# Performance work log

Measured on AMD Instinct MI355X. Metric: run time of the kernel, lower is better.

## Reference

```python
import jax, jax.numpy as jnp
import numpy as np

NUM_GROUPS = 32
EPS = 1e-5

def group_norm(x, weight, bias):
    # x: [B, C, H, W]
    b, c, h, w = x.shape
    g = NUM_GROUPS
    xg = x.reshape(b, g, (c // g) * h * w)
    mean = xg.mean(axis=-1, keepdims=True)
    var = xg.var(axis=-1, keepdims=True)
    xn = ((xg - mean) * jax.lax.rsqrt(var + EPS)).reshape(b, c, h, w)
    return xn * weight[None, :, None, None] + bias[None, :, None, None]

def setup_inputs() -> dict:
    key = jax.random.key(0)
    ks = jax.random.split(key, 4)
    B, C, H, W = 4, 256, 64, 64
    x = jax.random.normal(ks[0], (B, C, H, W), dtype=jnp.float32)
    gn_weight = jnp.ones((C,), dtype=jnp.float32)
    gn_bias = jnp.zeros((C,), dtype=jnp.float32)
    # 1x1 conv == linear over channel dim; init ~ kaiming-uniform-ish scale
    qkv_weight = jax.random.normal(ks[1], (3 * C, C), dtype=jnp.float32) / np.sqrt(C)
    qkv_bias = jnp.zeros((3 * C,), dtype=jnp.float32)
    out_weight = jax.random.normal(ks[2], (C, C), dtype=jnp.float32) / np.sqrt(C)
    out_bias = jnp.zeros((C,), dtype=jnp.float32)
    return {"x": x, "gn_weight": gn_weight, "gn_bias": gn_bias,
            "qkv_weight": qkv_weight, "qkv_bias": qkv_bias,
            "out_weight": out_weight, "out_bias": out_bias}

def reference(x, gn_weight, gn_bias, qkv_weight, qkv_bias, out_weight, out_bias):
    b, c, h, w = x.shape
    n = h * w
    xn = group_norm(x, gn_weight, gn_bias)
    # 1x1 conv QKV projection: [B, 3C, H, W]
    qkv = jnp.einsum('bchw,oc->bohw', xn, qkv_weight) + qkv_bias[None, :, None, None]
    q, k, v = jnp.split(qkv, 3, axis=1)
    q = q.transpose(0, 2, 3, 1).reshape(b, n, c)   # [B, N, C]
    k = k.reshape(b, c, n)                         # [B, C, N]
    v = v.transpose(0, 2, 3, 1).reshape(b, n, c)   # [B, N, C]
    scores = jnp.einsum('bnc,bcm->bnm', q, k) * (c ** -0.5)  # [B, N, N]
    attn = jax.nn.softmax(scores, axis=-1)
    out = jnp.einsum('bnm,bmc->bnc', attn, v)      # [B, N, C]
    out = out.reshape(b, h, w, c).transpose(0, 3, 1, 2)  # [B, C, H, W]
    out = jnp.einsum('bchw,oc->bohw', out, out_weight) + out_bias[None, :, None, None]
    return out + x
```

## Files before the change

### kernel.cpp

```cpp
#include <hip/hip_runtime.h>
#include <math.h>

#define B_   4
#define C_   256
#define G_   32
#define CPG  8
#define N_   4096
#define NPG  (CPG * N_)
#define EPS  1e-5f
#define SCALE 0.0625f

typedef __attribute__((ext_vector_type(8)))  __bf16 bf16x8;
typedef __attribute__((ext_vector_type(4)))  __bf16 bf16x4;
typedef __attribute__((ext_vector_type(16))) float  f32x16;

__global__ __launch_bounds__(256) void gn_stats_kernel(const float* __restrict__ x,
                                                       float* __restrict__ part) {
    int bid = blockIdx.x;
    int bg = bid >> 2, seg = bid & 3;
    const float4* xp4 = (const float4*)(x + (size_t)bg * NPG) + seg * 2048;
    int tid = threadIdx.x;

    float s = 0.f, ss = 0.f;
    for (int i = tid; i < 2048; i += 256) {
        float4 t = xp4[i];
        s  += t.x + t.y + t.z + t.w;
        ss += t.x * t.x + t.y * t.y + t.z * t.z + t.w * t.w;
    }
    #pragma unroll
    for (int off = 32; off; off >>= 1) {
        s  += __shfl_xor(s, off, 64);
        ss += __shfl_xor(ss, off, 64);
    }
    __shared__ float rs[2][4];
    int wave = tid >> 6, lane = tid & 63;
    if (lane == 0) { rs[0][wave] = s; rs[1][wave] = ss; }
    __syncthreads();
    if (tid == 0) {
        part[bid * 2]     = rs[0][0] + rs[0][1] + rs[0][2] + rs[0][3];
        part[bid * 2 + 1] = rs[1][0] + rs[1][1] + rs[1][2] + rs[1][3];
    }
}

__global__ __launch_bounds__(256) void gn_apply_kernel(const float* __restrict__ x,
                                                       const float* __restrict__ w,
                                                       const float* __restrict__ bia,
                                                       const float* __restrict__ part,
                                                       __bf16* __restrict__ xnb) {
    int bid = blockIdx.x;
    int bg = bid >> 4, seg = bid & 15;
    int b = bg >> 5, g = bg & 31;
    float s  = part[(bg * 4 + 0) * 2] + part[(bg * 4 + 1) * 2]
             + part[(bg * 4 + 2) * 2] + part[(bg * 4 + 3) * 2];
    float ss = part[(bg * 4 + 0) * 2 + 1] + part[(bg * 4 + 1) * 2 + 1]
             + part[(bg * 4 + 2) * 2 + 1] + part[(bg * 4 + 3) * 2 + 1];
    float mean = s / (float)NPG;
    float var  = ss / (float)NPG - mean * mean;
    float rstd = rsqrtf(var + EPS);

    const float* xp = x + (size_t)bg * NPG;
    int n = seg * 256 + threadIdx.x;

    bf16x8 pk;
    #pragma unroll
    for (int cc = 0; cc < 8; cc++) {
        float sc = rstd * w[g * CPG + cc];
        float sh = bia[g * CPG + cc] - mean * sc;
        pk[cc] = (__bf16)(xp[(size_t)cc * N_ + n] * sc + sh);
    }
    size_t idx = ((((size_t)(b * 128 + (n >> 5)) * 16 + (g >> 1)) * 2 + (g & 1))
                  * 32 + (n & 31)) * 8;
    *(bf16x8*)(xnb + idx) = pk;
}

__global__ __launch_bounds__(256) void qkv_kernel(const __bf16* __restrict__ xnb,
                                                  const float* __restrict__ W,
                                                  const float* __restrict__ bias,
                                                  __bf16* __restrict__ q,
                                                  __bf16* __restrict__ k,
                                                  __bf16* __restrict__ v) {
    int b = blockIdx.z, ot = blockIdx.y, nc = blockIdx.x;
    int tid = threadIdx.x, wv = tid >> 6, lane = tid & 63;
    int n31 = lane & 31, q2 = lane >> 5;
    int B0 = ot * 128 + wv * 32;

    bf16x8 wf[16];
    const float* wp = W + (size_t)(B0 + n31) * C_;
    #pragma unroll
    for (int ks = 0; ks < 16; ks++) {
        float4 t0 = *(const float4*)(wp + ks * 16 + q2 * 8);
        float4 t1 = *(const float4*)(wp + ks * 16 + q2 * 8 + 4);
        bf16x8 f;
        f[0] = (__bf16)t0.x; f[1] = (__bf16)t0.y; f[2] = (__bf16)t0.z; f[3] = (__bf16)t0.w;
        f[4] = (__bf16)t1.x; f[5] = (__bf16)t1.y; f[6] = (__bf16)t1.z; f[7] = (__bf16)t1.w;
        wf[ks] = f;
    }

    float bv[16], bvv = 0.f;
    if (ot < 4) {
        #pragma unroll
        for (int gI = 0; gI < 4; gI++)
            #pragma unroll
            for (int j = 0; j < 4; j++)
                bv[gI * 4 + j] = bias[B0 + gI * 8 + 4 * q2 + j];
    } else {
        bvv = bias[B0 + n31];
    }

    const __bf16* xb = xnb + (size_t)b * 128 * 8192;

    for (int t = 0; t < 4; t++) {
        int nt = nc * 4 + t;
        const __bf16* xg = xb + (size_t)nt * 8192 + q2 * 256 + n31 * 8;
        bf16x8 xf[16];
        #pragma unroll
        for (int ks = 0; ks < 16; ks++) xf[ks] = *(const bf16x8*)(xg + ks * 512);

        f32x16 acc;
        #pragma unroll
        for (int i = 0; i < 16; i++) acc[i] = 0.f;
        if (ot < 4) {
            #pragma unroll
            for (int ks = 0; ks < 16; ks++)
                acc = __builtin_amdgcn_mfma_f32_32x32x16_bf16(wf[ks], xf[ks], acc, 0, 0, 0);
        } else {
            #pragma unroll
            for (int ks = 0; ks < 16; ks++)
                acc = __builtin_amdgcn_mfma_f32_32x32x16_bf16(xf[ks], wf[ks], acc, 0, 0, 0);
        }

        if (ot < 4) {
            int ocb = (ot < 2) ? B0 : (B0 - 256);
            __bf16* dst = (ot < 2) ? q : k;
            bool isq = (ot < 2);
            #pragma unroll
            for (int gI = 0; gI < 4; gI++) {
                bf16x4 pk;
                #pragma unroll
                for (int j = 0; j < 4; j++) {
                    float y = acc[gI * 4 + j] + bv[gI * 4 + j];
                    if (isq) y *= SCALE;
                    pk[j] = (__bf16)y;
                }
                size_t idx = ((((size_t)(b * 128 + nt) * 16 + ((ocb >> 4) + (gI >> 1))) * 2
                               + (gI & 1)) * 32 + n31) * 8 + 4 * q2;
                *(bf16x4*)(dst + idx) = pk;
            }
        } else {
            int ocb = B0 - 512;
            #pragma unroll
            for (int gI = 0; gI < 4; gI++) {
                bf16x4 pk;
                #pragma unroll
                for (int j = 0; j < 4; j++)
                    pk[j] = (__bf16)(acc[gI * 4 + j] + bvv);
                size_t idx = (((((size_t)(b * 128 + nt) * 2 + (gI >> 1)) * 2 + (gI & 1)) * 8
                               + (ocb >> 5)) * 32 + n31) * 8 + 4 * q2;
                *(bf16x4*)(v + idx) = pk;
            }
        }
    }
}

#define PSTR 68

__global__ __launch_bounds__(512, 4) void attn_kernel(const __bf16* __restrict__ q,
                                                      const __bf16* __restrict__ k,
                                                      const __bf16* __restrict__ v,
                                                      float* __restrict__ ao0,
                                                      float* __restrict__ ao1,
                                                      float* __restrict__ l0,
                                                      float* __restrict__ l1) {
    __shared__ __bf16 p_lds[2][64 * PSTR];
    __shared__ float  l_lds[64];

    int bid   = blockIdx.x;
    int xcd   = bid & 7;
    int b     = xcd >> 1;
    int split = xcd & 1;
    int qt    = bid >> 3;
    int n0    = qt * 64;

    int tid = threadIdx.x;
    int wid = tid >> 6, lane = tid & 63;
    int n31 = lane & 31, q2 = lane >> 5;

    if (tid < 64) l_lds[tid] = 0.f;

    const size_t BSTR = (size_t)N_ * C_;

    if (wid < 4) {
        int kt = wid & 1;
        int rt = wid >> 1;
        const __bf16* qg = q + (size_t)(b * 128 + qt * 2 + rt) * 8192
                           + q2 * 256 + n31 * 8;
        bf16x8 qf[16];
        #pragma unroll
        for (int ks = 0; ks < 16; ks++) qf[ks] = *(const bf16x8*)(qg + ks * 512);

        const __bf16* kbase = k + (size_t)(b * 128 + split * 64 + kt) * 8192
                              + q2 * 256 + n31 * 8;
        float l_acc = 0.f;

        for (int ch = 0; ch < 32; ch++) {
            __syncthreads();
            const __bf16* kg = kbase + (size_t)ch * 16384;
            f32x16 s;
            #pragma unroll
            for (int i = 0; i < 16; i++) s[i] = 0.f;
            #pragma unroll
            for (int ks = 0; ks < 16; ks++) {
                bf16x8 kf = *(const bf16x8*)(kg + ks * 512);
                s = __builtin_amdgcn_mfma_f32_32x32x16_bf16(kf, qf[ks], s, 0, 0, 0);
            }
            __bf16* pbuf = p_lds[ch & 1];
            #pragma unroll
            for (int g = 0; g < 4; g++) {
                bf16x4 pw;
                #pragma unroll
                for (int j = 0; j < 4; j++) {
                    float p = __expf(s[g * 4 + j]);
                    l_acc += p;
                    pw[j] = (__bf16)p;
                }
                *(bf16x4*)(pbuf + (rt * 32 + n31) * PSTR + kt * 32 + 8 * g + 4 * q2) = pw;
            }
        }
        atomicAdd(&l_lds[rt * 32 + n31], l_acc);
        __syncthreads();
        if (tid < 64) {
            float* lp = split ? l1 : l0;
            lp[(size_t)b * N_ + n0 + tid] = l_lds[tid];
        }
    } else {
        int cw = wid - 4;
        const __bf16* vbase = v + (size_t)b * BSTR + (size_t)split * 524288
                              + (size_t)q2 * 2048 + n31 * 8;
        f32x16 o_acc[2][2];
        #pragma unroll
        for (int ct = 0; ct < 2; ct++)
            #pragma unroll
            for (int rt = 0; rt < 2; rt++)
                #pragma unroll
                for (int i = 0; i < 16; i++) o_acc[ct][rt][i] = 0.f;

        for (int ch = 0; ch < 32; ch++) {
            __syncthreads();
            if (ch > 0) {
                int cc = ch - 1;
                const __bf16* pbuf = p_lds[cc & 1];
                #pragma unroll
                for (int ct = 0; ct < 2; ct++) {
                    bf16x8 vf[4];
                    #pragma unroll
                    for (int ks4 = 0; ks4 < 4; ks4++) {
                        size_t off = (size_t)(cc * 2 + (ks4 >> 1)) * 8192
                                   + (size_t)(ks4 & 1) * 4096 + (cw * 2 + ct) * 256;
                        vf[ks4] = *(const bf16x8*)(vbase + off);
                    }
                    #pragma unroll
                    for (int rt = 0; rt < 2; rt++) {
                        const __bf16* pb = pbuf + (rt * 32 + n31) * PSTR + q2 * 8;
                        #pragma unroll
                        for (int ks4 = 0; ks4 < 4; ks4++) {
                            bf16x8 pf = *(const bf16x8*)(pb + ks4 * 16);
                            o_acc[ct][rt] = __builtin_amdgcn_mfma_f32_32x32x16_bf16(
                                vf[ks4], pf, o_acc[ct][rt], 0, 0, 0);
                        }
                    }
                }
            }
        }
        __syncthreads();
        {
            int cc = 31;
            const __bf16* pbuf = p_lds[1];
            #pragma unroll
            for (int ct = 0; ct < 2; ct++) {
                bf16x8 vf[4];
                #pragma unroll
                for (int ks4 = 0; ks4 < 4; ks4++) {
                    size_t off = (size_t)(cc * 2 + (ks4 >> 1)) * 8192
                               + (size_t)(ks4 & 1) * 4096 + (cw * 2 + ct) * 256;
                    vf[ks4] = *(const bf16x8*)(vbase + off);
                }
                #pragma unroll
                for (int rt = 0; rt < 2; rt++) {
                    const __bf16* pb = pbuf + (rt * 32 + n31) * PSTR + q2 * 8;
                    #pragma unroll
                    for (int ks4 = 0; ks4 < 4; ks4++) {
                        bf16x8 pf = *(const bf16x8*)(pb + ks4 * 16);
                        o_acc[ct][rt] = __builtin_amdgcn_mfma_f32_32x32x16_bf16(
                            vf[ks4], pf, o_acc[ct][rt], 0, 0, 0);
                    }
                }
            }
        }
        float* aop = split ? ao1 : ao0;
        #pragma unroll
        for (int ct = 0; ct < 2; ct++)
            #pragma unroll
            for (int rt = 0; rt < 2; rt++)
                #pragma unroll
                for (int g = 0; g < 4; g++) {
                    float4 st;
                    st.x = o_acc[ct][rt][g * 4 + 0];
                    st.y = o_acc[ct][rt][g * 4 + 1];
                    st.z = o_acc[ct][rt][g * 4 + 2];
                    st.w = o_acc[ct][rt][g * 4 + 3];
                    size_t idx = ((((((size_t)(b * 64 + qt) * 4 + cw) * 2 + ct) * 2 + rt)
                                   * 4 + g) * 2 + q2) * 128 + n31 * 4;
                    *(float4*)(aop + idx) = st;
                }
    }
}

__global__ __launch_bounds__(256) void proj_kernel(const float* __restrict__ ao0,
                                                   const float* __restrict__ ao1,
                                                   const float* __restrict__ l0p,
                                                   const float* __restrict__ l1p,
                                                   const float* __restrict__ W2,
                                                   const float* __restrict__ bias,
                                                   const float* __restrict__ x,
                                                   float* __restrict__ out) {
    int b = blockIdx.z, ot = blockIdx.y, nc = blockIdx.x;
    int tid = threadIdx.x, wv = tid >> 6, lane = tid & 63;
    int n31 = lane & 31, q2 = lane >> 5;
    int B0 = ot * 128 + wv * 32;

    bf16x8 wf[16];
    const float* wp = W2 + (size_t)(B0 + n31) * C_;
    #pragma unroll
    for (int ks = 0; ks < 16; ks++) {
        float4 t0 = *(const float4*)(wp + ks * 16 + q2 * 8);
        float4 t1 = *(const float4*)(wp + ks * 16 + q2 * 8 + 4);
        bf16x8 f;
        f[0] = (__bf16)t0.x; f[1] = (__bf16)t0.y; f[2] = (__bf16)t0.z; f[3] = (__bf16)t0.w;
        f[4] = (__bf16)t1.x; f[5] = (__bf16)t1.y; f[6] = (__bf16)t1.z; f[7] = (__bf16)t1.w;
        wf[ks] = f;
    }
    float bv[16];
    #pragma unroll
    for (int r = 0; r < 16; r++) bv[r] = bias[B0 + (r & 3) + 8 * (r >> 2) + 4 * q2];

    for (int t = 0; t < 4; t++) {
        int nt = nc * 4 + t;
        int qt = nt >> 1, rtile = nt & 1;
        int n = nt * 32 + n31;
        float inv = 1.0f / (l0p[(size_t)b * N_ + n] + l1p[(size_t)b * N_ + n]);

        bf16x8 xf[16];
        #pragma unroll
        for (int ks = 0; ks < 16; ks++) {
            int oct = ks * 2 + q2;
            int cw = oct >> 3, ct = (oct >> 2) & 1, ga = oct & 3;
            size_t base = ((((((size_t)(b * 64 + qt) * 4 + cw) * 2 + ct) * 2 + rtile)
                            * 4 + ga) * 2) * 128 + n31 * 4;
            float4 a0 = *(const float4*)(ao0 + base);
            float4 b0 = *(const float4*)(ao0 + base + 128);
            float4 a1 = *(const float4*)(ao1 + base);
            float4 b1 = *(const float4*)(ao1 + base + 128);
            bf16x8 f;
            f[0] = (__bf16)((a0.x + a1.x) * inv);
            f[1] = (__bf16)((a0.y + a1.y) * inv);
            f[2] = (__bf16)((a0.z + a1.z) * inv);
            f[3] = (__bf16)((a0.w + a1.w) * inv);
            f[4] = (__bf16)((b0.x + b1.x) * inv);
            f[5] = (__bf16)((b0.y + b1.y) * inv);
            f[6] = (__bf16)((b0.z + b1.z) * inv);
            f[7] = (__bf16)((b0.w + b1.w) * inv);
            xf[ks] = f;
        }

        f32x16 acc;
        #pragma unroll
        for (int i = 0; i < 16; i++) acc[i] = 0.f;
        #pragma unroll
        for (int ks = 0; ks < 16; ks++)
            acc = __builtin_amdgcn_mfma_f32_32x32x16_bf16(wf[ks], xf[ks], acc, 0, 0, 0);

        #pragma unroll
        for (int r = 0; r < 16; r++) {
            int o = B0 + (r & 3) + 8 * (r >> 2) + 4 * q2;
            size_t idx = ((size_t)(b * C_ + o)) * N_ + nt * 32 + n31;
            out[idx] = acc[r] + bv[r] + x[idx];
        }
    }
}

extern "C" void kernel_launch(void* const* d_in, const int* in_sizes, int n_in,
                              void* d_out, int out_size, void* d_ws, size_t ws_size,
                              hipStream_t stream) {
    const float* x     = (const float*)d_in[0];
    const float* gn_w  = (const float*)d_in[1];
    const float* gn_b  = (const float*)d_in[2];
    const float* qkv_w = (const float*)d_in[3];
    const float* qkv_b = (const float*)d_in[4];
    const float* out_w = (const float*)d_in[5];
    const float* out_b = (const float*)d_in[6];
    float* out = (float*)d_out;

    const size_t SZ = (size_t)B_ * C_ * N_;
    char* base = (char*)d_ws;
    float*  ao0 = (float*)base;
    float*  ao1 = (float*)(base + SZ * 4);
    __bf16* xnb = (__bf16*)base;
    __bf16* qb  = (__bf16*)(base + 2 * SZ * 4);
    __bf16* kb  = qb + SZ;
    __bf16* vb  = kb + SZ;
    float*  l0  = (float*)(base + 2 * SZ * 4 + 3 * SZ * 2);
    float*  l1  = l0 + B_ * N_;
    float*  part = l1 + B_ * N_;

    gn_stats_kernel<<<dim3(512), 256, 0, stream>>>(x, part);
    gn_apply_kernel<<<dim3(2048), 256, 0, stream>>>(x, gn_w, gn_b, part, xnb);
    qkv_kernel<<<dim3(32, 6, B_), 256, 0, stream>>>(xnb, qkv_w, qkv_b, qb, kb, vb);
    attn_kernel<<<dim3(512), 512, 0, stream>>>(qb, kb, vb, ao0, ao1, l0, l1);
    proj_kernel<<<dim3(32, 2, B_), 256, 0, stream>>>(ao0, ao1, l0, l1, out_w, out_b, x, out);
}
```

Before: 229.7 us.

## Stage K tiles in LDS via async global_load_lds and single-buffer P

The score waves now stream each K chunk into a double-buffered LDS tile using global_load_lds. The two waves that share a key tile read it from LDS, which halves global K traffic. The P buffer becomes single-buffered, and the PV waves no longer lag one chunk behind: each iteration loads V, waits on a second barrier, then consumes the current P. This drops the one-chunk skew between the QK and PV wave groups, so the two phases may serialize. The extra 64 KB of LDS also cuts how many blocks fit on a CU below the launch-bounds target.

```diff
diff --git a/kernel.cpp b/kernel.cpp
--- a/kernel.cpp
+++ b/kernel.cpp
@@ -171,7 +171,8 @@
                                                       float* __restrict__ ao1,
                                                       float* __restrict__ l0,
                                                       float* __restrict__ l1) {
-    __shared__ __bf16 p_lds[2][64 * PSTR];
+    __shared__ __bf16 k_lds[2][16384];
+    __shared__ __bf16 p_lds[64 * PSTR];
     __shared__ float  l_lds[64];
 
     int bid   = blockIdx.x;
@@ -198,22 +199,30 @@
         #pragma unroll
         for (int ks = 0; ks < 16; ks++) qf[ks] = *(const bf16x8*)(qg + ks * 512);
 
-        const __bf16* kbase = k + (size_t)(b * 128 + split * 64 + kt) * 8192
-                              + q2 * 256 + n31 * 8;
+        const __bf16* kchunk0 = k + (size_t)(b * 128 + split * 64) * 8192;
         float l_acc = 0.f;
+
+        {
+            const __bf16* src = kchunk0 + wid * 4096 + lane * 8;
+            __bf16* dst = &k_lds[0][wid * 4096];
+            #pragma unroll
+            for (int i = 0; i < 8; i++)
+                __builtin_amdgcn_global_load_lds(
+                    (const __attribute__((address_space(1))) void*)(src + i * 512),
+                    (__attribute__((address_space(3))) void*)(dst + i * 512), 16, 0, 0);
+        }
 
         for (int ch = 0; ch < 32; ch++) {
             __syncthreads();
-            const __bf16* kg = kbase + (size_t)ch * 16384;
+            const __bf16* klds = &k_lds[ch & 1][kt * 8192];
             f32x16 s;
             #pragma unroll
             for (int i = 0; i < 16; i++) s[i] = 0.f;
             #pragma unroll
             for (int ks = 0; ks < 16; ks++) {
-                bf16x8 kf = *(const bf16x8*)(kg + ks * 512);
+                bf16x8 kf = *(const bf16x8*)(klds + ks * 512 + lane * 8);
                 s = __builtin_amdgcn_mfma_f32_32x32x16_bf16(kf, qf[ks], s, 0, 0, 0);
             }
-            __bf16* pbuf = p_lds[ch & 1];
             #pragma unroll
             for (int g = 0; g < 4; g++) {
                 bf16x4 pw;
@@ -223,7 +232,17 @@
                     l_acc += p;
                     pw[j] = (__bf16)p;
                 }
-                *(bf16x4*)(pbuf + (rt * 32 + n31) * PSTR + kt * 32 + 8 * g + 4 * q2) = pw;
+                *(bf16x4*)(p_lds + (rt * 32 + n31) * PSTR + kt * 32 + 8 * g + 4 * q2) = pw;
+            }
+            __syncthreads();
+            if (ch + 1 < 32) {
+                const __bf16* src = kchunk0 + (size_t)(ch + 1) * 16384 + wid * 4096 + lane * 8;
+                __bf16* dst = &k_lds[(ch + 1) & 1][wid * 4096];
+                #pragma unroll
+                for (int i = 0; i < 8; i++)
+                    __builtin_amdgcn_global_load_lds(
+                        (const __attribute__((address_space(1))) void*)(src + i * 512),
+                        (__attribute__((address_space(3))) void*)(dst + i * 512), 16, 0, 0);
             }
         }
         atomicAdd(&l_lds[rt * 32 + n31], l_acc);
@@ -246,56 +265,32 @@
 
         for (int ch = 0; ch < 32; ch++) {
             __syncthreads();
-            if (ch > 0) {
-                int cc = ch - 1;
-                const __bf16* pbuf = p_lds[cc & 1];
-                #pragma unroll
-                for (int ct = 0; ct < 2; ct++) {
-                    bf16x8 vf[4];
+            bf16x8 vf[2][4];
+            #pragma unroll
+            for (int ct = 0; ct < 2; ct++)
+                #pragma unroll
+                for (int ks4 = 0; ks4 < 4; ks4++) {
+                    size_t off = (size_t)(ch * 2 + (ks4 >> 1)) * 8192
+                               + (size_t)(ks4 & 1) * 4096 + (cw * 2 + ct) * 256;
+                    vf[ct][ks4] = *(const bf16x8*)(vbase + off);
+                }
+            __syncthreads();
+            #pragma unroll
+            for (int rt = 0; rt < 2; rt++) {
+                bf16x8 pf[4];
+                const __bf16* pb = p_lds + (rt * 32 + n31) * PSTR + q2 * 8;
+                #pragma unroll
+                for (int ks4 = 0; ks4 < 4; ks4++)
+                    pf[ks4] = *(const bf16x8*)(pb + ks4 * 16);
+                #pragma unroll
+                for (int ct = 0; ct < 2; ct++)
                     #pragma unroll
-                    for (int ks4 = 0; ks4 < 4; ks4++) {
-                        size_t off = (size_t)(cc * 2 + (ks4 >> 1)) * 8192
-                                   + (size_t)(ks4 & 1) * 4096 + (cw * 2 + ct) * 256;
-                        vf[ks4] = *(const bf16x8*)(vbase + off);
-                    }
-                    #pragma unroll
-                    for (int rt = 0; rt < 2; rt++) {
-                        const __bf16* pb = pbuf + (rt * 32 + n31) * PSTR + q2 * 8;
-                        #pragma unroll
-                        for (int ks4 = 0; ks4 < 4; ks4++) {
-                            bf16x8 pf = *(const bf16x8*)(pb + ks4 * 16);
-                            o_acc[ct][rt] = __builtin_amdgcn_mfma_f32_32x32x16_bf16(
-                                vf[ks4], pf, o_acc[ct][rt], 0, 0, 0);
-                        }
-                    }
-                }
+                    for (int ks4 = 0; ks4 < 4; ks4++)
+                        o_acc[ct][rt] = __builtin_amdgcn_mfma_f32_32x32x16_bf16(
+                            vf[ct][ks4], pf[ks4], o_acc[ct][rt], 0, 0, 0);
             }
         }
         __syncthreads();
-        {
-            int cc = 31;
-            const __bf16* pbuf = p_lds[1];
-            #pragma unroll
-            for (int ct = 0; ct < 2; ct++) {
-                bf16x8 vf[4];
-                #pragma unroll
-                for (int ks4 = 0; ks4 < 4; ks4++) {
-                    size_t off = (size_t)(cc * 2 + (ks4 >> 1)) * 8192
-                               + (size_t)(ks4 & 1) * 4096 + (cw * 2 + ct) * 256;
-                    vf[ks4] = *(const bf16x8*)(vbase + off);
-                }
-                #pragma unroll
-                for (int rt = 0; rt < 2; rt++) {
-                    const __bf16* pb = pbuf + (rt * 32 + n31) * PSTR + q2 * 8;
-                    #pragma unroll
-                    for (int ks4 = 0; ks4 < 4; ks4++) {
-                        bf16x8 pf = *(const bf16x8*)(pb + ks4 * 16);
-                        o_acc[ct][rt] = __builtin_amdgcn_mfma_f32_32x32x16_bf16(
-                            vf[ks4], pf, o_acc[ct][rt], 0, 0, 0);
-                    }
-                }
-            }
-        }
         float* aop = split ? ao1 : ao0;
         #pragma unroll
         for (int ct = 0; ct < 2; ct++)
```

Measured after the change: 232.5 us. Within noise of the previous version (+1.2%).
